# Kernel optimization log

Hardware: AMD Instinct MI355X
Metric: run time of the kernel (lower is better)

The kernel has to match this reference:

```python
import jax, jax.numpy as jnp
import numpy as np

B, T, SD, AD, E, H, L, FF, MS = 8, 512, 17, 6, 512, 8, 3, 2048, 4096
S3 = 3 * T  # interleaved sequence length
D = E // H
EPS = 1e-5


def _layernorm(x, g, b):
    m = jnp.mean(x, axis=-1, keepdims=True)
    v = jnp.mean((x - m) ** 2, axis=-1, keepdims=True)
    return (x - m) * jax.lax.rsqrt(v + EPS) * g + b


def setup_inputs() -> dict:
    key = jax.random.key(0)
    ks = jax.random.split(key, 24)
    sc = 0.02

    def rn(k, shape):
        return (jax.random.normal(k, shape, jnp.float32) * sc).astype(jnp.float32)

    inp = {
        'state': jax.random.normal(ks[0], (B, T, SD), jnp.float32),
        'action': jax.random.normal(ks[1], (B, T, AD), jnp.float32),
        'reward': jax.random.normal(ks[2], (B, T, 1), jnp.float32),
        'timestep': jax.random.randint(ks[3], (B, T), 0, MS),
        # embeddings
        'sW': rn(ks[4], (SD, E)), 'sb': jnp.zeros((E,), jnp.float32),
        'aW': rn(ks[5], (AD, E)), 'ab': jnp.zeros((E,), jnp.float32),
        'rW': rn(ks[6], (1, E)), 'rb': jnp.zeros((E,), jnp.float32),
        'temb': rn(ks[7], (MS, E)),
        'lnE_g': jnp.ones((E,), jnp.float32), 'lnE_b': jnp.zeros((E,), jnp.float32),
        # transformer blocks, stacked over depth L
        'qW': rn(ks[8], (L, E, E)), 'qb': jnp.zeros((L, E), jnp.float32),
        'kW': rn(ks[9], (L, E, E)), 'kb': jnp.zeros((L, E), jnp.float32),
        'vW': rn(ks[10], (L, E, E)), 'vb': jnp.zeros((L, E), jnp.float32),
        'pW': rn(ks[11], (L, E, E)), 'pb': jnp.zeros((L, E), jnp.float32),
        'ln1_g': jnp.ones((L, E), jnp.float32), 'ln1_b': jnp.zeros((L, E), jnp.float32),
        'm1W': rn(ks[12], (L, E, FF)), 'm1b': jnp.zeros((L, FF), jnp.float32),
        'm2W': rn(ks[13], (L, FF, E)), 'm2b': jnp.zeros((L, E), jnp.float32),
        'ln2_g': jnp.ones((L, E), jnp.float32), 'ln2_b': jnp.zeros((L, E), jnp.float32),
        # prediction heads
        'hdR_W': rn(ks[14], (E, 1)), 'hdR_b': jnp.zeros((1,), jnp.float32),
        'hdS_W': rn(ks[15], (E, SD)), 'hdS_b': jnp.zeros((SD,), jnp.float32),
        'hdA_W': rn(ks[16], (E, AD)), 'hdA_b': jnp.zeros((AD,), jnp.float32),
    }
    return inp


def _forward(state, action, reward, timestep, p):
    te = p['temb'][timestep]  # [B,T,E]
    se = state @ p['sW'] + p['sb'] + te
    ae = action @ p['aW'] + p['ab'] + te
    re = reward @ p['rW'] + p['rb'] + te
    # interleave (return, state, action) per timestep -> [B, 3T, E]
    h = jnp.stack((re, se, ae), axis=2).reshape(B, S3, E)
    h = _layernorm(h, p['lnE_g'], p['lnE_b'])

    causal = jnp.tril(jnp.ones((S3, S3), bool))
    scale = 1.0 / jnp.sqrt(jnp.float32(D))
    for i in range(L):
        q = (h @ p['qW'][i] + p['qb'][i]).reshape(B, S3, H, D).transpose(0, 2, 1, 3)
        k = (h @ p['kW'][i] + p['kb'][i]).reshape(B, S3, H, D).transpose(0, 2, 1, 3)
        v = (h @ p['vW'][i] + p['vb'][i]).reshape(B, S3, H, D).transpose(0, 2, 1, 3)
        w = jnp.einsum('bhqd,bhkd->bhqk', q, k) * scale
        w = jnp.where(causal, w, -jnp.inf)
        att = jnp.einsum('bhqk,bhkd->bhqd', jax.nn.softmax(w, axis=-1), v)
        att = att.transpose(0, 2, 1, 3).reshape(B, S3, E)
        h = h + (att @ p['pW'][i] + p['pb'][i])
        h = _layernorm(h, p['ln1_g'][i], p['ln1_b'][i])
        m = jax.nn.gelu(h @ p['m1W'][i] + p['m1b'][i], approximate=False)
        h = h + (m @ p['m2W'][i] + p['m2b'][i])
        h = _layernorm(h, p['ln2_g'][i], p['ln2_b'][i])

    h = h.reshape(B, T, 3, E).transpose(0, 2, 1, 3)  # [B,3,T,E]
    h_state, h_action = h[:, 1], h[:, 2]
    return_preds = h_action @ p['hdR_W'] + p['hdR_b']
    state_preds = h_action @ p['hdS_W'] + p['hdS_b']
    action_preds = jnp.tanh(h_state @ p['hdA_W'] + p['hdA_b'])
    return state_preds, action_preds, return_preds


def reference(state, action, reward, timestep, sW, sb, aW, ab, rW, rb, temb,
              lnE_g, lnE_b, qW, qb, kW, kb, vW, vb, pW, pb, ln1_g, ln1_b,
              m1W, m1b, m2W, m2b, ln2_g, ln2_b, hdR_W, hdR_b, hdS_W, hdS_b,
              hdA_W, hdA_b):
    p = dict(sW=sW, sb=sb, aW=aW, ab=ab, rW=rW, rb=rb, temb=temb,
             lnE_g=lnE_g, lnE_b=lnE_b, qW=qW, qb=qb, kW=kW, kb=kb, vW=vW,
             vb=vb, pW=pW, pb=pb, ln1_g=ln1_g, ln1_b=ln1_b, m1W=m1W,
             m1b=m1b, m2W=m2W, m2b=m2b, ln2_g=ln2_g, ln2_b=ln2_b,
             hdR_W=hdR_W, hdR_b=hdR_b, hdS_W=hdS_W, hdS_b=hdS_b,
             hdA_W=hdA_W, hdA_b=hdA_b)
    return _forward(state, action, reward, timestep, p)
```

## Files before the change

### kernel.cpp

```cpp
#include <hip/hip_runtime.h>
#include <hip/hip_bf16.h>


#define S3 1536
#define EMB 512
#define NROWS 12288
#define NTOK 4096
#define QKV_STR 1536
#define QSCALE 0.18033688f
#define WT_L 3145728

typedef __hip_bfloat16 bf16;
typedef __attribute__((ext_vector_type(8))) short short8;
typedef __attribute__((ext_vector_type(4))) float f32x4;

__device__ inline float bf2f(bf16 b) { return __bfloat162float(b); }
__device__ inline bf16 f2bf(float f) { return __float2bfloat16(f); }
__device__ inline unsigned short f2bfu(float f) {
    bf16 h = __float2bfloat16(f);
    return *reinterpret_cast<unsigned short*>(&h);
}
__device__ inline float bfu2f(unsigned short v) {
    bf16 h = *reinterpret_cast<bf16*>(&v);
    return __bfloat162float(h);
}
__device__ inline float fast_gelu(float v) {
    float u = v * fmaf(v * v, 0.0356774081f, 0.7978845608f);
    return v * __builtin_amdgcn_rcpf(1.0f + exp2f(u * -2.885390082f));
}

__device__ inline void gload_lds16(const void* g, void* lds) {
    __builtin_amdgcn_global_load_lds(
        (const __attribute__((address_space(1))) void*)g,
        (__attribute__((address_space(3))) void*)lds, 16, 0, 0);
}

__global__ __launch_bounds__(256) void embed_v9(
    const float* __restrict__ state, const float* __restrict__ action,
    const float* __restrict__ reward, const int* __restrict__ timestep,
    const float* __restrict__ sW, const float* __restrict__ sb,
    const float* __restrict__ aW, const float* __restrict__ ab,
    const float* __restrict__ rW, const float* __restrict__ rb,
    const float* __restrict__ temb, bf16* __restrict__ hb)
{
    int tok = blockIdx.x;
    int b = tok >> 9;
    int t = tok & 511;
    int tid = threadIdx.x;
    int ts = timestep[tok];
    long hbase = ((long)b * S3 + 3L * t) * EMB;
    const float* st = state + (long)tok * 17;
    const float* ac = action + (long)tok * 6;
    float rw = reward[tok];
    float sv[17], av[6];
#pragma unroll
    for (int j = 0; j < 17; ++j) sv[j] = st[j];
#pragma unroll
    for (int j = 0; j < 6; ++j) av[j] = ac[j];
    for (int c = tid; c < EMB; c += 256) {
        float te = temb[(long)ts * EMB + c];
        float re = rw * rW[c] + rb[c] + te;
        float se = sb[c] + te;
#pragma unroll
        for (int j = 0; j < 17; ++j) se = fmaf(sv[j], sW[j * EMB + c], se);
        float ae = ab[c] + te;
#pragma unroll
        for (int j = 0; j < 6; ++j) ae = fmaf(av[j], aW[j * EMB + c], ae);
        hb[hbase + c] = f2bf(re);
        hb[hbase + EMB + c] = f2bf(se);
        hb[hbase + 2 * EMB + c] = f2bf(ae);
    }
}

__global__ __launch_bounds__(256) void addln_v13(
    bf16* __restrict__ hb, const bf16* __restrict__ delta,
    const float* __restrict__ g, const float* __restrict__ bb, int hasDelta)
{
    int tid = threadIdx.x;
    int w = tid >> 6, l = tid & 63;
    long row = (long)blockIdx.x * 4 + w;
    long base = row * EMB + l * 8;
    short8 xv = *reinterpret_cast<const short8*>(&hb[base]);
    float x[8];
#pragma unroll
    for (int j = 0; j < 8; ++j) x[j] = bfu2f((unsigned short)xv[j]);
    if (hasDelta) {
        short8 dv = *reinterpret_cast<const short8*>(&delta[base]);
#pragma unroll
        for (int j = 0; j < 8; ++j) x[j] += bfu2f((unsigned short)dv[j]);
    }
    float s = 0.f;
#pragma unroll
    for (int j = 0; j < 8; ++j) s += x[j];
#pragma unroll
    for (int off = 32; off; off >>= 1) s += __shfl_xor(s, off);
    float mean = s * (1.0f / EMB);
    float vs = 0.f;
#pragma unroll
    for (int j = 0; j < 8; ++j) { x[j] -= mean; vs += x[j] * x[j]; }
#pragma unroll
    for (int off = 32; off; off >>= 1) vs += __shfl_xor(vs, off);
    float rstd = rsqrtf(vs * (1.0f / EMB) + 1e-5f);
    float4 g0 = *reinterpret_cast<const float4*>(&g[l * 8]);
    float4 g1 = *reinterpret_cast<const float4*>(&g[l * 8 + 4]);
    float4 c0 = *reinterpret_cast<const float4*>(&bb[l * 8]);
    float4 c1 = *reinterpret_cast<const float4*>(&bb[l * 8 + 4]);
    short8 o;
    o[0] = (short)f2bfu(x[0] * rstd * g0.x + c0.x);
    o[1] = (short)f2bfu(x[1] * rstd * g0.y + c0.y);
    o[2] = (short)f2bfu(x[2] * rstd * g0.z + c0.z);
    o[3] = (short)f2bfu(x[3] * rstd * g0.w + c0.w);
    o[4] = (short)f2bfu(x[4] * rstd * g1.x + c1.x);
    o[5] = (short)f2bfu(x[5] * rstd * g1.y + c1.y);
    o[6] = (short)f2bfu(x[6] * rstd * g1.z + c1.z);
    o[7] = (short)f2bfu(x[7] * rstd * g1.w + c1.w);
    *reinterpret_cast<short8*>(&hb[base]) = o;
}

__global__ __launch_bounds__(256) void transp_v12(
    const float* __restrict__ qW, const float* __restrict__ kW,
    const float* __restrict__ vW, const float* __restrict__ pW,
    const float* __restrict__ m1W, const float* __restrict__ m2W,
    short* __restrict__ WtAll)
{
    __shared__ short tile[64][68];
    int bid0 = blockIdx.x, t = threadIdx.x;
    int layer = bid0 / 768;
    int bid = bid0 - layer * 768;
    const long we = (long)layer * EMB * EMB;
    const long wm1 = (long)layer * EMB * 2048;
    short* Wt = WtAll + (long)layer * WT_L;
    const float* W; short* Dt; int K, N, nkt, tl;
    if (bid < 192)      { int w = bid / 64; tl = bid % 64;
                          W = ((w == 0) ? qW : (w == 1) ? kW : vW) + we;
                          Dt = Wt + w * 262144; K = 512; N = 512; nkt = 8; }
    else if (bid < 256) { tl = bid - 192; W = pW + we;  Dt = Wt + 786432;  K = 512;  N = 512;  nkt = 8; }
    else if (bid < 512) { tl = bid - 256; W = m1W + wm1; Dt = Wt + 1048576; K = 512;  N = 2048; nkt = 8; }
    else                { tl = bid - 512; W = m2W + wm1; Dt = Wt + 2097152; K = 2048; N = 512;  nkt = 32; }
    int k0 = (tl % nkt) * 64, n0 = (tl / nkt) * 64;
    int c = t & 63, r4 = t >> 6;
#pragma unroll
    for (int p = 0; p < 16; ++p) {
        int r = r4 + p * 4;
        tile[r][c] = (short)f2bfu(W[(long)(k0 + r) * N + n0 + c]);
    }
    __syncthreads();
#pragma unroll
    for (int p = 0; p < 16; ++p) {
        int rr = r4 + p * 4;
        Dt[(long)(n0 + rr) * K + k0 + c] = tile[c][rr];
    }
}

template <int BM>
__global__ __launch_bounds__(256) void gemm_v16(
    const bf16* __restrict__ A, const short* __restrict__ Wt,
    const float* __restrict__ b0, const float* __restrict__ b1,
    const float* __restrict__ b2, bf16* __restrict__ C,
    bf16* __restrict__ VT,
    int N, int K, int nbx, int act, int bsplit)
{
    constexpr int NF = (BM == 128) ? 4 : 2;
    constexpr int AC = BM / 32;
    __shared__ short As[BM * 64];
    __shared__ short Bs[128 * 64];
    int t = threadIdx.x;
    int nb = gridDim.x;
    int bid = blockIdx.x;
    bid = (bid & 7) * (nb >> 3) + (bid >> 3);
    int row0 = (bid / nbx) * BM;
    int col0 = (bid % nbx) * 128;
    int wid = t >> 6, l = t & 63;
    int wm = (BM == 128) ? (wid >> 1) : 0;
    int wn = (BM == 128) ? (wid & 1) : wid;
    int l15 = l & 15, l4 = l >> 4;
    int lrow = l >> 3, lslot = l & 7;

    f32x4 acc[4][NF] = {};

    for (int k0 = 0; k0 < K; k0 += 64) {
#pragma unroll
        for (int c = 0; c < AC; ++c) {
            int chunk = wid * AC + c;
            int row = chunk * 8 + lrow;
            int gs = lslot ^ (row & 7);
            gload_lds16(&A[(long)(row0 + row) * K + k0 + gs * 8], &As[chunk * 512]);
        }
#pragma unroll
        for (int c = 0; c < 4; ++c) {
            int chunk = wid * 4 + c;
            int row = chunk * 8 + lrow;
            int gs = lslot ^ (row & 7);
            gload_lds16(&Wt[(long)(col0 + row) * K + k0 + gs * 8], &Bs[chunk * 512]);
        }
        __syncthreads();
#pragma unroll
        for (int ks = 0; ks < 2; ++ks) {
            short8 af[4], bfr[NF];
#pragma unroll
            for (int m = 0; m < 4; ++m) {
                int r = wm * 64 + m * 16 + l15;
                af[m] = *reinterpret_cast<const short8*>(&As[r * 64 + (((ks * 4 + l4) ^ (r & 7)) * 8)]);
            }
#pragma unroll
            for (int n = 0; n < NF; ++n) {
                int r = wn * (NF * 16) + n * 16 + l15;
                bfr[n] = *reinterpret_cast<const short8*>(&Bs[r * 64 + (((ks * 4 + l4) ^ (r & 7)) * 8)]);
            }
#pragma unroll
            for (int m = 0; m < 4; ++m)
#pragma unroll
                for (int n = 0; n < NF; ++n)
                    acc[m][n] = __builtin_amdgcn_mfma_f32_16x16x32_bf16(bfr[n], af[m], acc[m][n], 0, 0, 0);
        }
        __syncthreads();
    }
    bool vblock = (bsplit && col0 >= 1024);
#pragma unroll
    for (int m = 0; m < 4; ++m) {
        int row = row0 + wm * 64 + m * 16 + l15;
#pragma unroll
        for (int n = 0; n < NF; ++n) {
            int col = col0 + wn * (NF * 16) + n * 16 + l4 * 4;
            const float* bp = bsplit ? (col < 512 ? &b0[col] : col < 1024 ? &b1[col - 512] : &b2[col - 1024])
                                     : &b0[col];
            float4 bv = *reinterpret_cast<const float4*>(bp);
            float qs = (bsplit && col < 512) ? QSCALE : 1.0f;
            float v0 = (acc[m][n][0] + bv.x) * qs;
            float v1 = (acc[m][n][1] + bv.y) * qs;
            float v2 = (acc[m][n][2] + bv.z) * qs;
            float v3 = (acc[m][n][3] + bv.w) * qs;
            if (act) {
                v0 = fast_gelu(v0);
                v1 = fast_gelu(v1);
                v2 = fast_gelu(v2);
                v3 = fast_gelu(v3);
            }
            if (vblock) {
                int b = row / S3;
                int s = row - b * S3;
                int hhd = col - 1024;
                long vbase = ((long)(b * 8 + (hhd >> 6)) * 64 + (hhd & 63)) * S3 + s;
                VT[vbase]          = f2bf(v0);
                VT[vbase + S3]     = f2bf(v1);
                VT[vbase + 2 * S3] = f2bf(v2);
                VT[vbase + 3 * S3] = f2bf(v3);
            } else {
                ushort4 o;
                o.x = f2bfu(v0); o.y = f2bfu(v1); o.z = f2bfu(v2); o.w = f2bfu(v3);
                *reinterpret_cast<ushort4*>(&C[(long)row * N + col]) = o;
            }
        }
    }
}

__global__ __launch_bounds__(256) void flash_v16(
    const bf16* __restrict__ QKV, const bf16* __restrict__ VT,
    bf16* __restrict__ O)
{
    __shared__ short QPs[4096], Ks[2][4096], Vs[2][4096];
    int t = threadIdx.x;
    int bid = blockIdx.x;
    int qb = 23 - (bid >> 6);
    int bh = bid & 63;
    int b = bh >> 3, hh = bh & 7;
    long baseq = (long)b * S3 * QKV_STR + hh * 64;
    long basev = (long)bh * 64 * S3;
    long baseo = (long)b * S3 * EMB + hh * 64;
    int q0 = qb * 64;
    int wid = t >> 6, l = t & 63;
    int l15 = l & 15, l4 = l >> 4;
    int lrow = l >> 3, lslot = l & 7;

#pragma unroll
    for (int c = 0; c < 2; ++c) {
        int chunk = c * 4 + wid;
        int row = chunk * 8 + lrow;
        int gs = lslot ^ (row & 7);
        gload_lds16(&QKV[baseq + (long)(q0 + row) * QKV_STR + gs * 8], &QPs[chunk * 512]);
    }
#pragma unroll
    for (int c = 0; c < 2; ++c) {
        int chunk = c * 4 + wid;
        int row = chunk * 8 + lrow;
        int gs = lslot ^ (row & 7);
        gload_lds16(&QKV[baseq + 512 + (long)row * QKV_STR + gs * 8], &Ks[0][chunk * 512]);
        gload_lds16(&VT[basev + (long)row * S3 + gs * 8], &Vs[0][chunk * 512]);
    }
    asm volatile("s_waitcnt vmcnt(4)" ::: "memory");
    __builtin_amdgcn_s_barrier();
    short8 qf[2];
    {
        int rq = wid * 16 + l15;
#pragma unroll
        for (int ks = 0; ks < 2; ++ks)
            qf[ks] = *reinterpret_cast<const short8*>(&QPs[rq * 64 + (((ks * 4 + l4) ^ (rq & 7)) * 8)]);
    }
    asm volatile("s_waitcnt lgkmcnt(0)" ::: "memory");

    f32x4 oacc[4] = {};
    float li = 0.f;

    for (int kt = 0; kt <= qb; ++kt) {
        int cur = kt & 1;
        if (kt < qb) {
            int k1 = (kt + 1) * 64;
#pragma unroll
            for (int c = 0; c < 2; ++c) {
                int chunk = c * 4 + wid;
                int row = chunk * 8 + lrow;
                int gs = lslot ^ (row & 7);
                gload_lds16(&QKV[baseq + 512 + (long)(k1 + row) * QKV_STR + gs * 8], &Ks[cur ^ 1][chunk * 512]);
                gload_lds16(&VT[basev + (long)row * S3 + k1 + gs * 8], &Vs[cur ^ 1][chunk * 512]);
            }
            asm volatile("s_waitcnt vmcnt(4)" ::: "memory");
        } else {
            asm volatile("s_waitcnt vmcnt(0)" ::: "memory");
        }
        __builtin_amdgcn_s_barrier();
        __builtin_amdgcn_sched_barrier(0);

        f32x4 s[4] = {};
        __builtin_amdgcn_s_setprio(1);
#pragma unroll
        for (int ks = 0; ks < 2; ++ks) {
#pragma unroll
            for (int n = 0; n < 4; ++n) {
                int rk = n * 16 + l15;
                short8 kf = *reinterpret_cast<const short8*>(&Ks[cur][rk * 64 + (((ks * 4 + l4) ^ (rk & 7)) * 8)]);
                s[n] = __builtin_amdgcn_mfma_f32_16x16x32_bf16(kf, qf[ks], s[n], 0, 0, 0);
            }
        }
        __builtin_amdgcn_s_setprio(0);
        if (kt == qb) {
            int qloc = wid * 16 + l15;
#pragma unroll
            for (int n = 0; n < 4; ++n) {
#pragma unroll
                for (int r = 0; r < 4; ++r)
                    if (n * 16 + l4 * 4 + r > qloc) s[n][r] = -1e30f;
            }
        }
        float rs = 0.f;
#pragma unroll
        for (int n = 0; n < 4; ++n)
#pragma unroll
            for (int r = 0; r < 4; ++r) {
                float p = exp2f(s[n][r]);
                s[n][r] = p;
                rs += p;
            }
        rs += __shfl_xor(rs, 16);
        rs += __shfl_xor(rs, 32);
        li += rs;
        {
            int qrow = wid * 16 + l15;
#pragma unroll
            for (int n = 0; n < 4; ++n) {
                ushort4 pk;
                pk.x = f2bfu(s[n][0]); pk.y = f2bfu(s[n][1]);
                pk.z = f2bfu(s[n][2]); pk.w = f2bfu(s[n][3]);
                int slot = n * 2 + (l4 >> 1);
                *reinterpret_cast<ushort4*>(
                    &QPs[qrow * 64 + ((slot ^ (qrow & 7)) * 8) + (l4 & 1) * 4]) = pk;
            }
        }
        __builtin_amdgcn_s_setprio(1);
#pragma unroll
        for (int ks = 0; ks < 2; ++ks) {
            int prow = wid * 16 + l15;
            short8 pa = *reinterpret_cast<const short8*>(
                &QPs[prow * 64 + (((ks * 4 + l4) ^ (prow & 7)) * 8)]);
#pragma unroll
            for (int n = 0; n < 4; ++n) {
                int rk = n * 16 + l15;
                short8 vb = *reinterpret_cast<const short8*>(&Vs[cur][rk * 64 + (((ks * 4 + l4) ^ (rk & 7)) * 8)]);
                oacc[n] = __builtin_amdgcn_mfma_f32_16x16x32_bf16(pa, vb, oacc[n], 0, 0, 0);
            }
        }
        __builtin_amdgcn_s_setprio(0);
        asm volatile("s_waitcnt lgkmcnt(0)" ::: "memory");
        __builtin_amdgcn_s_barrier();
    }
    float lir[4];
#pragma unroll
    for (int r = 0; r < 4; ++r)
        lir[r] = __shfl(li, (l & 48) | (l4 * 4 + r));
    int rowb = q0 + wid * 16 + l4 * 4;
#pragma unroll
    for (int n = 0; n < 4; ++n) {
        int col = n * 16 + l15;
#pragma unroll
        for (int r = 0; r < 4; ++r)
            O[baseo + (long)(rowb + r) * EMB + col] = f2bf(oacc[n][r] / lir[r]);
    }
}

__global__ __launch_bounds__(256) void heads_v13(
    const bf16* __restrict__ hb,
    const float* __restrict__ hdR_W, const float* __restrict__ hdR_b,
    const float* __restrict__ hdS_W, const float* __restrict__ hdS_b,
    const float* __restrict__ hdA_W, const float* __restrict__ hdA_b,
    float* __restrict__ out)
{
    __shared__ short rows[16][512];
    int tid = threadIdx.x;
    int tok0 = blockIdx.x * 8;
#pragma unroll
    for (int p = 0; p < 4; ++p) {
        int i = p * 256 + tid;
        int rowIdx = i >> 6;
        int seg = i & 63;
        int tk = rowIdx >> 1, which = rowIdx & 1;
        int tokg = tok0 + tk;
        int b = tokg >> 9, tt = tokg & 511;
        long gaddr = ((long)b * S3 + 3L * tt + 1 + which) * EMB + seg * 8;
        *reinterpret_cast<short8*>(&rows[rowIdx][seg * 8]) =
            *reinterpret_cast<const short8*>(&hb[gaddr]);
    }
    __syncthreads();
    int o = tid >> 3, g = tid & 7;
    if (o >= 24) return;
    int which = (o >= 17 && o < 23) ? 0 : 1;
    float wreg[64];
#pragma unroll
    for (int i2 = 0; i2 < 64; ++i2) {
        int kk = g * 64 + i2;
        wreg[i2] = (o < 17) ? hdS_W[kk * 17 + o]
                 : (o < 23) ? hdA_W[kk * 6 + (o - 17)]
                            : hdR_W[kk];
    }
#pragma unroll
    for (int tk = 0; tk < 8; ++tk) {
        const short* src = &rows[tk * 2 + which][g * 64];
        float sum = 0.f;
#pragma unroll
        for (int i2 = 0; i2 < 8; ++i2) {
            short8 v = *reinterpret_cast<const short8*>(&src[i2 * 8]);
#pragma unroll
            for (int j = 0; j < 8; ++j)
                sum = fmaf(bfu2f((unsigned short)v[j]), wreg[i2 * 8 + j], sum);
        }
        sum += __shfl_xor(sum, 1);
        sum += __shfl_xor(sum, 2);
        sum += __shfl_xor(sum, 4);
        if (g == 0) {
            int tokg = tok0 + tk;
            if (o < 17)       out[(long)tokg * 17 + o] = sum + hdS_b[o];
            else if (o < 23)  out[69632 + (long)tokg * 6 + (o - 17)] = tanhf(sum + hdA_b[o - 17]);
            else              out[94208 + tokg] = sum + hdR_b[0];
        }
    }
}

extern "C" void kernel_launch(void* const* d_in, const int* in_sizes, int n_in,
                              void* d_out, int out_size, void* d_ws, size_t ws_size,
                              hipStream_t stream) {
    const float* state   = (const float*)d_in[0];
    const float* action  = (const float*)d_in[1];
    const float* reward  = (const float*)d_in[2];
    const int*   timestep= (const int*)  d_in[3];
    const float* sW   = (const float*)d_in[4];
    const float* sb   = (const float*)d_in[5];
    const float* aW   = (const float*)d_in[6];
    const float* ab   = (const float*)d_in[7];
    const float* rW   = (const float*)d_in[8];
    const float* rb   = (const float*)d_in[9];
    const float* temb = (const float*)d_in[10];
    const float* lnE_g= (const float*)d_in[11];
    const float* lnE_b= (const float*)d_in[12];
    const float* qW   = (const float*)d_in[13];
    const float* qb_  = (const float*)d_in[14];
    const float* kW   = (const float*)d_in[15];
    const float* kb_  = (const float*)d_in[16];
    const float* vW   = (const float*)d_in[17];
    const float* vb_  = (const float*)d_in[18];
    const float* pW   = (const float*)d_in[19];
    const float* pb_  = (const float*)d_in[20];
    const float* ln1_g= (const float*)d_in[21];
    const float* ln1_b= (const float*)d_in[22];
    const float* m1W  = (const float*)d_in[23];
    const float* m1b  = (const float*)d_in[24];
    const float* m2W  = (const float*)d_in[25];
    const float* m2b  = (const float*)d_in[26];
    const float* ln2_g= (const float*)d_in[27];
    const float* ln2_b= (const float*)d_in[28];
    const float* hdR_W= (const float*)d_in[29];
    const float* hdR_b= (const float*)d_in[30];
    const float* hdS_W= (const float*)d_in[31];
    const float* hdS_b= (const float*)d_in[32];
    const float* hdA_W= (const float*)d_in[33];
    const float* hdA_b= (const float*)d_in[34];

    if (ws_size < 94371840u) return;
    char* wsb = (char*)d_ws;
    bf16* hb   = (bf16*)wsb;
    bf16* qkv  = (bf16*)(wsb + 12582912);
    bf16* att  = (bf16*)(wsb + 50331648);
    bf16* xb   = (bf16*)(wsb + 62914560);
    bf16* vT   = xb;
    bf16* m    = qkv;
    short* Wt  = (short*)(wsb + 75497472);

    embed_v9<<<NTOK, 256, 0, stream>>>(state, action, reward, timestep,
                                       sW, sb, aW, ab, rW, rb, temb, hb);
    addln_v13<<<NROWS / 4, 256, 0, stream>>>(hb, nullptr, lnE_g, lnE_b, 0);
    transp_v12<<<3 * 768, 256, 0, stream>>>(qW, kW, vW, pW, m1W, m2W, Wt);

    for (int i = 0; i < 3; ++i) {
        short* Wl = Wt + (long)i * WT_L;
        gemm_v16<64><<<192 * 12, 256, 0, stream>>>(hb, Wl, qb_ + i * EMB, kb_ + i * EMB,
                                                   vb_ + i * EMB, qkv, vT, 1536, 512, 12, 0, 1);
        flash_v16<<<24 * 64, 256, 0, stream>>>(qkv, vT, att);
        gemm_v16<64><<<192 * 4, 256, 0, stream>>>(att, Wl + 786432, pb_ + i * EMB,
                                                  nullptr, nullptr, xb, nullptr, 512, 512, 4, 0, 0);
        addln_v13<<<NROWS / 4, 256, 0, stream>>>(hb, xb, ln1_g + i * EMB, ln1_b + i * EMB, 1);
        gemm_v16<128><<<96 * 16, 256, 0, stream>>>(hb, Wl + 1048576, m1b + i * 2048,
                                                   nullptr, nullptr, m, nullptr, 2048, 512, 16, 1, 0);
        gemm_v16<64><<<192 * 4, 256, 0, stream>>>(m, Wl + 2097152, m2b + i * EMB,
                                                  nullptr, nullptr, xb, nullptr, 512, 2048, 4, 0, 0);
        addln_v13<<<NROWS / 4, 256, 0, stream>>>(hb, xb, ln2_g + i * EMB, ln2_b + i * EMB, 1);
    }

    heads_v13<<<NTOK / 8, 256, 0, stream>>>(hb, hdR_W, hdR_b, hdS_W, hdS_b,
                                            hdA_W, hdA_b, (float*)d_out);
}
```

Measured before the change: 666.1 us.

## Double-buffer GEMM LDS tiles and drop flash setprio hints

Rewrites the GEMM kernel to double-buffer the A and B shared-memory tiles, prefetching the next K-slice with async global-to-LDS loads while MFMAs run on the current one, using explicit vmcnt waits and raw barriers. It removes the 128-row template variant, so the MLP up-projection now uses 64-row tiles with twice as many blocks. It also removes the s_setprio hints around the MFMA sections in the flash attention kernel. The intent is to hide global load latency in the GEMMs; the cost is doubled LDS use per block (48KB), which may reduce occupancy, and less B-tile reuse for the FF1 GEMM.

Result: faster. 647.1 us (-2.9%).

```diff
diff --git a/kernel.cpp b/kernel.cpp
--- a/kernel.cpp
+++ b/kernel.cpp
@@ -152,76 +152,85 @@
     }
 }
 
-template <int BM>
-__global__ __launch_bounds__(256) void gemm_v16(
+__global__ __launch_bounds__(256) void gemm_v17(
     const bf16* __restrict__ A, const short* __restrict__ Wt,
     const float* __restrict__ b0, const float* __restrict__ b1,
     const float* __restrict__ b2, bf16* __restrict__ C,
     bf16* __restrict__ VT,
     int N, int K, int nbx, int act, int bsplit)
 {
-    constexpr int NF = (BM == 128) ? 4 : 2;
-    constexpr int AC = BM / 32;
-    __shared__ short As[BM * 64];
-    __shared__ short Bs[128 * 64];
+    __shared__ short As[2][64 * 64];
+    __shared__ short Bs[2][128 * 64];
     int t = threadIdx.x;
     int nb = gridDim.x;
     int bid = blockIdx.x;
     bid = (bid & 7) * (nb >> 3) + (bid >> 3);
-    int row0 = (bid / nbx) * BM;
+    int row0 = (bid / nbx) * 64;
     int col0 = (bid % nbx) * 128;
     int wid = t >> 6, l = t & 63;
-    int wm = (BM == 128) ? (wid >> 1) : 0;
-    int wn = (BM == 128) ? (wid & 1) : wid;
     int l15 = l & 15, l4 = l >> 4;
     int lrow = l >> 3, lslot = l & 7;
-
-    f32x4 acc[4][NF] = {};
-
-    for (int k0 = 0; k0 < K; k0 += 64) {
-#pragma unroll
-        for (int c = 0; c < AC; ++c) {
-            int chunk = wid * AC + c;
+    int kn = K >> 6;
+
+    f32x4 acc[4][2] = {};
+
+    auto stage = [&](int buf, int k0) {
+#pragma unroll
+        for (int c = 0; c < 2; ++c) {
+            int chunk = wid * 2 + c;
             int row = chunk * 8 + lrow;
             int gs = lslot ^ (row & 7);
-            gload_lds16(&A[(long)(row0 + row) * K + k0 + gs * 8], &As[chunk * 512]);
+            gload_lds16(&A[(long)(row0 + row) * K + k0 + gs * 8], &As[buf][chunk * 512]);
         }
 #pragma unroll
         for (int c = 0; c < 4; ++c) {
             int chunk = wid * 4 + c;
             int row = chunk * 8 + lrow;
             int gs = lslot ^ (row & 7);
-            gload_lds16(&Wt[(long)(col0 + row) * K + k0 + gs * 8], &Bs[chunk * 512]);
-        }
-        __syncthreads();
+            gload_lds16(&Wt[(long)(col0 + row) * K + k0 + gs * 8], &Bs[buf][chunk * 512]);
+        }
+    };
+
+    stage(0, 0);
+    for (int kt = 0; kt < kn; ++kt) {
+        int cur = kt & 1;
+        if (kt + 1 < kn) {
+            stage(cur ^ 1, (kt + 1) * 64);
+            asm volatile("s_waitcnt vmcnt(6)" ::: "memory");
+        } else {
+            asm volatile("s_waitcnt vmcnt(0)" ::: "memory");
+        }
+        __builtin_amdgcn_s_barrier();
+        __builtin_amdgcn_sched_barrier(0);
 #pragma unroll
         for (int ks = 0; ks < 2; ++ks) {
-            short8 af[4], bfr[NF];
+            short8 af[4], bfr[2];
 #pragma unroll
             for (int m = 0; m < 4; ++m) {
-                int r = wm * 64 + m * 16 + l15;
-                af[m] = *reinterpret_cast<const short8*>(&As[r * 64 + (((ks * 4 + l4) ^ (r & 7)) * 8)]);
-            }
-#pragma unroll
-            for (int n = 0; n < NF; ++n) {
-                int r = wn * (NF * 16) + n * 16 + l15;
-                bfr[n] = *reinterpret_cast<const short8*>(&Bs[r * 64 + (((ks * 4 + l4) ^ (r & 7)) * 8)]);
+                int r = m * 16 + l15;
+                af[m] = *reinterpret_cast<const short8*>(&As[cur][r * 64 + (((ks * 4 + l4) ^ (r & 7)) * 8)]);
+            }
+#pragma unroll
+            for (int n = 0; n < 2; ++n) {
+                int r = wid * 32 + n * 16 + l15;
+                bfr[n] = *reinterpret_cast<const short8*>(&Bs[cur][r * 64 + (((ks * 4 + l4) ^ (r & 7)) * 8)]);
             }
 #pragma unroll
             for (int m = 0; m < 4; ++m)
 #pragma unroll
-                for (int n = 0; n < NF; ++n)
+                for (int n = 0; n < 2; ++n)
                     acc[m][n] = __builtin_amdgcn_mfma_f32_16x16x32_bf16(bfr[n], af[m], acc[m][n], 0, 0, 0);
         }
-        __syncthreads();
+        asm volatile("s_waitcnt lgkmcnt(0)" ::: "memory");
+        __builtin_amdgcn_s_barrier();
     }
     bool vblock = (bsplit && col0 >= 1024);
 #pragma unroll
     for (int m = 0; m < 4; ++m) {
-        int row = row0 + wm * 64 + m * 16 + l15;
-#pragma unroll
-        for (int n = 0; n < NF; ++n) {
-            int col = col0 + wn * (NF * 16) + n * 16 + l4 * 4;
+        int row = row0 + m * 16 + l15;
+#pragma unroll
+        for (int n = 0; n < 2; ++n) {
+            int col = col0 + wid * 32 + n * 16 + l4 * 4;
             const float* bp = bsplit ? (col < 512 ? &b0[col] : col < 1024 ? &b1[col - 512] : &b2[col - 1024])
                                      : &b0[col];
             float4 bv = *reinterpret_cast<const float4*>(bp);
@@ -254,7 +263,7 @@
     }
 }
 
-__global__ __launch_bounds__(256) void flash_v16(
+__global__ __launch_bounds__(256) void flash_v17(
     const bf16* __restrict__ QKV, const bf16* __restrict__ VT,
     bf16* __restrict__ O)
 {
@@ -321,7 +330,6 @@
         __builtin_amdgcn_sched_barrier(0);
 
         f32x4 s[4] = {};
-        __builtin_amdgcn_s_setprio(1);
 #pragma unroll
         for (int ks = 0; ks < 2; ++ks) {
 #pragma unroll
@@ -331,7 +339,6 @@
                 s[n] = __builtin_amdgcn_mfma_f32_16x16x32_bf16(kf, qf[ks], s[n], 0, 0, 0);
             }
         }
-        __builtin_amdgcn_s_setprio(0);
         if (kt == qb) {
             int qloc = wid * 16 + l15;
 #pragma unroll
@@ -365,7 +372,6 @@
                     &QPs[qrow * 64 + ((slot ^ (qrow & 7)) * 8) + (l4 & 1) * 4]) = pk;
             }
         }
-        __builtin_amdgcn_s_setprio(1);
 #pragma unroll
         for (int ks = 0; ks < 2; ++ks) {
             int prow = wid * 16 + l15;
@@ -378,7 +384,6 @@
                 oacc[n] = __builtin_amdgcn_mfma_f32_16x16x32_bf16(pa, vb, oacc[n], 0, 0, 0);
             }
         }
-        __builtin_amdgcn_s_setprio(0);
         asm volatile("s_waitcnt lgkmcnt(0)" ::: "memory");
         __builtin_amdgcn_s_barrier();
     }
@@ -509,16 +514,16 @@
 
     for (int i = 0; i < 3; ++i) {
         short* Wl = Wt + (long)i * WT_L;
-        gemm_v16<64><<<192 * 12, 256, 0, stream>>>(hb, Wl, qb_ + i * EMB, kb_ + i * EMB,
-                                                   vb_ + i * EMB, qkv, vT, 1536, 512, 12, 0, 1);
-        flash_v16<<<24 * 64, 256, 0, stream>>>(qkv, vT, att);
-        gemm_v16<64><<<192 * 4, 256, 0, stream>>>(att, Wl + 786432, pb_ + i * EMB,
-                                                  nullptr, nullptr, xb, nullptr, 512, 512, 4, 0, 0);
+        gemm_v17<<<192 * 12, 256, 0, stream>>>(hb, Wl, qb_ + i * EMB, kb_ + i * EMB,
+                                               vb_ + i * EMB, qkv, vT, 1536, 512, 12, 0, 1);
+        flash_v17<<<24 * 64, 256, 0, stream>>>(qkv, vT, att);
+        gemm_v17<<<192 * 4, 256, 0, stream>>>(att, Wl + 786432, pb_ + i * EMB,
+                                              nullptr, nullptr, xb, nullptr, 512, 512, 4, 0, 0);
         addln_v13<<<NROWS / 4, 256, 0, stream>>>(hb, xb, ln1_g + i * EMB, ln1_b + i * EMB, 1);
-        gemm_v16<128><<<96 * 16, 256, 0, stream>>>(hb, Wl + 1048576, m1b + i * 2048,
-                                                   nullptr, nullptr, m, nullptr, 2048, 512, 16, 1, 0);
-        gemm_v16<64><<<192 * 4, 256, 0, stream>>>(m, Wl + 2097152, m2b + i * EMB,
-                                                  nullptr, nullptr, xb, nullptr, 512, 2048, 4, 0, 0);
+        gemm_v17<<<192 * 16, 256, 0, stream>>>(hb, Wl + 1048576, m1b + i * 2048,
+                                               nullptr, nullptr, m, nullptr, 2048, 512, 16, 1, 0);
+        gemm_v17<<<192 * 4, 256, 0, stream>>>(m, Wl + 2097152, m2b + i * EMB,
+                                              nullptr, nullptr, xb, nullptr, 512, 2048, 4, 0, 0);
         addln_v13<<<NROWS / 4, 256, 0, stream>>>(hb, xb, ln2_g + i * EMB, ln2_b + i * EMB, 1);
     }
 
```
